# Kernel optimization log

Measured on AMD Instinct MI355X. Metric: run time of the kernel, lower is better.

The kernel has to match this reference:

```python
import jax, jax.numpy as jnp
import numpy as np

IGNORE_INDEX = -100


def setup_inputs() -> dict:
    key = jax.random.key(0)
    k1, k2, k3 = jax.random.split(key, 3)
    VOCAB, D = 32000, 2048
    B, S = 4, 2048
    weight = jax.random.normal(k1, (VOCAB, D), dtype=jnp.float32) * 0.02
    hidden = jax.random.normal(k2, (B, S, D), dtype=jnp.float32)
    targets = jax.random.randint(k3, (B, S), 0, VOCAB, dtype=jnp.int64)
    return {"weight": weight, "hidden": hidden, "targets": targets}


def reference(weight, hidden, targets):
    # Fused linear + cross-entropy: loss = sum_t CE(hidden_t @ W^T, target_t) / n_valid.
    # (The torch module chunks over sequence purely to save memory; the math is
    # identical to the unchunked computation below.)
    B, S, D = hidden.shape
    flat_h = hidden.reshape(-1, D)            # [B*S, D]
    flat_t = targets.reshape(-1)              # [B*S]
    logits = (flat_h @ weight.T).astype(jnp.float32)  # [B*S, V]
    lse = jax.nn.logsumexp(logits, axis=-1)   # [B*S]
    safe_t = jnp.clip(flat_t, 0, logits.shape[-1] - 1)
    tgt_logit = jnp.take_along_axis(logits, safe_t[:, None], axis=-1)[:, 0]
    valid = flat_t != IGNORE_INDEX
    per_tok = jnp.where(valid, lse - tgt_logit, 0.0)
    total_loss = per_tok.sum()
    n_valid = valid.sum().astype(jnp.float32)
    return jnp.where(n_valid > 0, total_loss / n_valid, total_loss)
```

## Files before the change

kernel.cpp:

```cpp
#include <hip/hip_runtime.h>

#define IGNORE_INDEX (-100)
#define VOCAB 32000
#define DDIM  2048
#define MTOK  8192

#define BM 128
#define BN 128
#define BK 128

#define WSCALE 32.0f
#define HSCALE 8.0f
#define INVSCALE (1.0f / 256.0f)
#define SCALE_ONE 0x7F7F7F7F

#define WBLK ((VOCAB * DDIM) / (256 * 16))
#define HBLK ((MTOK * DDIM) / (256 * 16))

typedef float f32x4 __attribute__((ext_vector_type(4)));
typedef int   i32x8 __attribute__((ext_vector_type(8)));
typedef unsigned char uchar_t;

__device__ __forceinline__ void cvt16(const float4* __restrict__ src,
                                      int4* __restrict__ dst, float scale,
                                      size_t i) {
    float4 a = src[4 * i], b = src[4 * i + 1], c = src[4 * i + 2], d = src[4 * i + 3];
    int4 o;
    int v;
    v = 0;
    v = __builtin_amdgcn_cvt_pk_fp8_f32(a.x * scale, a.y * scale, v, false);
    v = __builtin_amdgcn_cvt_pk_fp8_f32(a.z * scale, a.w * scale, v, true);
    o.x = v;
    v = 0;
    v = __builtin_amdgcn_cvt_pk_fp8_f32(b.x * scale, b.y * scale, v, false);
    v = __builtin_amdgcn_cvt_pk_fp8_f32(b.z * scale, b.w * scale, v, true);
    o.y = v;
    v = 0;
    v = __builtin_amdgcn_cvt_pk_fp8_f32(c.x * scale, c.y * scale, v, false);
    v = __builtin_amdgcn_cvt_pk_fp8_f32(c.z * scale, c.w * scale, v, true);
    o.z = v;
    v = 0;
    v = __builtin_amdgcn_cvt_pk_fp8_f32(d.x * scale, d.y * scale, v, false);
    v = __builtin_amdgcn_cvt_pk_fp8_f32(d.z * scale, d.w * scale, v, true);
    o.w = v;
    dst[i] = o;
}

__global__ void cvt_f32_fp8(const float4* __restrict__ srcW, int4* __restrict__ dstW,
                            const float4* __restrict__ srcH, int4* __restrict__ dstH) {
    if (blockIdx.x < WBLK) {
        size_t i = (size_t)blockIdx.x * blockDim.x + threadIdx.x;
        cvt16(srcW, dstW, WSCALE, i);
    } else {
        size_t i = (size_t)(blockIdx.x - WBLK) * blockDim.x + threadIdx.x;
        cvt16(srcH, dstH, HSCALE, i);
    }
}

__device__ __forceinline__ void load_lds16(const uchar_t* g, uchar_t* l) {
    __builtin_amdgcn_global_load_lds(
        (const __attribute__((address_space(1))) unsigned int*)(const void*)g,
        (__attribute__((address_space(3))) unsigned int*)(void*)l,
        16, 0, 0);
}

__global__ __launch_bounds__(256, 4) void gemm_ce(
    const uchar_t* __restrict__ A,
    const uchar_t* __restrict__ B,
    const int* __restrict__ targets,
    float* __restrict__ sumexp,
    float* __restrict__ tgtlogit) {
    __shared__ alignas(16) uchar_t As[BM * BK];
    __shared__ alignas(16) uchar_t Bs[BN * BK];

    const int tid  = threadIdx.x;
    const int wave = tid >> 6;
    const int lane = tid & 63;
    const int quad = lane >> 4;
    const int l16  = lane & 15;
    const int wm   = (wave >> 1) * 64;
    const int wn   = (wave & 1) * 64;

    const int m0 = blockIdx.x * BM;
    const int n0 = blockIdx.y * BN;

    const int srow = lane >> 3;
    const int scol = ((((lane & 7) >> 1) ^ (srow & 3)) << 5) + ((lane & 1) << 4);

    const uchar_t* Ap = A + (size_t)(m0 + wave * 32 + srow) * DDIM + scol;
    const uchar_t* Bp = B + (size_t)(n0 + wave * 32 + srow) * DDIM + scol;
    uchar_t* AsW = &As[(wave * 32) * BK];
    uchar_t* BsW = &Bs[(wave * 32) * BK];

    f32x4 acc[4][4];
    const f32x4 zero = {0.f, 0.f, 0.f, 0.f};
#pragma unroll
    for (int i = 0; i < 4; ++i)
#pragma unroll
        for (int j = 0; j < 4; ++j) acc[i][j] = zero;

#pragma clang loop unroll(disable)
    for (int k0 = 0; k0 < DDIM; k0 += BK) {
#pragma unroll
        for (int it = 0; it < 4; ++it) {
            load_lds16(Ap + (size_t)it * 8 * DDIM + k0, AsW + it * 8 * BK);
            load_lds16(Bp + (size_t)it * 8 * DDIM + k0, BsW + it * 8 * BK);
        }
        __syncthreads();

        const int gsw = ((quad ^ (l16 & 3)) << 5);
        i32x8 af[4];
#pragma unroll
        for (int i = 0; i < 4; ++i)
            af[i] = *reinterpret_cast<const i32x8*>(
                &As[(wm + i * 16 + l16) * BK + gsw]);
#pragma unroll
        for (int j = 0; j < 4; ++j) {
            const i32x8 bf = *reinterpret_cast<const i32x8*>(
                &Bs[(wn + j * 16 + l16) * BK + gsw]);
#pragma unroll
            for (int i = 0; i < 4; ++i)
                acc[i][j] = __builtin_amdgcn_mfma_scale_f32_16x16x128_f8f6f4(
                    af[i], bf, acc[i][j],
                    0 , 0 ,
                    0, SCALE_ONE, 0, SCALE_ONE);
        }
        __syncthreads();
    }

#pragma unroll
    for (int i = 0; i < 4; ++i) {
#pragma unroll
        for (int r = 0; r < 4; ++r) {
            const int mg = m0 + wm + i * 16 + quad * 4 + r;
            const int t  = targets[mg];
            float p = 0.f;
#pragma unroll
            for (int j = 0; j < 4; ++j) {
                float v = acc[i][j][r] * INVSCALE;
                p += __expf(v);
                if (t == n0 + wn + j * 16 + l16) tgtlogit[mg] = v;
            }
            p += __shfl_xor(p, 1);
            p += __shfl_xor(p, 2);
            p += __shfl_xor(p, 4);
            p += __shfl_xor(p, 8);
            if (l16 == 0) atomicAdd(&sumexp[mg], p);
        }
    }
}

__global__ void finalize(const float* __restrict__ sumexp,
                         const float* __restrict__ tgtlogit,
                         const int* __restrict__ targets,
                         float* __restrict__ out) {
    __shared__ float s_sum[8];
    __shared__ float s_cnt[8];
    float local = 0.f, cnt = 0.f;
    for (int t = threadIdx.x; t < MTOK; t += blockDim.x) {
        int tg = targets[t];
        if (tg != IGNORE_INDEX) {
            local += logf(sumexp[t]) - tgtlogit[t];
            cnt += 1.f;
        }
    }
#pragma unroll
    for (int o = 32; o > 0; o >>= 1) {
        local += __shfl_down(local, o);
        cnt   += __shfl_down(cnt, o);
    }
    const int wave = threadIdx.x >> 6, lane = threadIdx.x & 63;
    if (lane == 0) { s_sum[wave] = local; s_cnt[wave] = cnt; }
    __syncthreads();
    if (threadIdx.x == 0) {
        float ts = 0.f, tc = 0.f;
        for (int w = 0; w < (int)(blockDim.x >> 6); ++w) {
            ts += s_sum[w];
            tc += s_cnt[w];
        }
        out[0] = (tc > 0.f) ? (ts / tc) : ts;
    }
}

extern "C" void kernel_launch(void* const* d_in, const int* in_sizes, int n_in,
                              void* d_out, int out_size, void* d_ws,
                              size_t ws_size, hipStream_t stream) {
    const float* weight  = (const float*)d_in[0];
    const float* hidden  = (const float*)d_in[1];
    const int*   targets = (const int*)d_in[2];
    float* out = (float*)d_out;

    const size_t wbytes = (size_t)VOCAB * DDIM;
    const size_t hbytes = (size_t)MTOK * DDIM;
    uchar_t* Wb = (uchar_t*)d_ws;
    uchar_t* Hb = (uchar_t*)d_ws + wbytes;
    float* sumexp   = (float*)((char*)d_ws + wbytes + hbytes);
    float* tgtlogit = sumexp + MTOK;

    cvt_f32_fp8<<<WBLK + HBLK, 256, 0, stream>>>(
        (const float4*)weight, (int4*)Wb, (const float4*)hidden, (int4*)Hb);

    hipMemsetAsync(sumexp, 0, 2 * MTOK * sizeof(float), stream);

    dim3 grid(MTOK / BM, VOCAB / BN);
    gemm_ce<<<grid, 256, 0, stream>>>(Hb, Wb, targets, sumexp, tgtlogit);

    finalize<<<1, 512, 0, stream>>>(sumexp, tgtlogit, targets, out);
}
```

Baseline: 975.2 us.

## Triple-buffer LDS pipeline with 256x128 tiles, 8 waves, and block-level sumexp reduction

The GEMM moves to 256x128 tiles with 512 threads and a three-stage LDS ring. Global-to-LDS prefetch is issued two K-steps ahead and gated by explicit vmcnt waits and barriers, so memory latency overlaps the MFMAs. Other changes: a new 16-byte XOR swizzle with split fragment reads, s_setprio around the MFMA block, and an LDS reduction of per-row sumexp before one atomic per row. The memset is folded into the conversion kernel and finalize uses 1024 threads. LDS use rises to 144KB per block, which may cap occupancy at one block per CU despite launch_bounds(512,2).

```diff
diff --git a/kernel.cpp b/kernel.cpp
--- a/kernel.cpp
+++ b/kernel.cpp
@@ -5,9 +5,10 @@
 #define DDIM  2048
 #define MTOK  8192
 
-#define BM 128
+#define BM 256
 #define BN 128
 #define BK 128
+#define NKT (DDIM / BK)
 
 #define WSCALE 32.0f
 #define HSCALE 8.0f
@@ -16,6 +17,7 @@
 
 #define WBLK ((VOCAB * DDIM) / (256 * 16))
 #define HBLK ((MTOK * DDIM) / (256 * 16))
+#define ZBLK ((2 * MTOK * 4) / (256 * 16))
 
 typedef float f32x4 __attribute__((ext_vector_type(4)));
 typedef int   i32x8 __attribute__((ext_vector_type(8)));
@@ -47,13 +49,17 @@
 }
 
 __global__ void cvt_f32_fp8(const float4* __restrict__ srcW, int4* __restrict__ dstW,
-                            const float4* __restrict__ srcH, int4* __restrict__ dstH) {
+                            const float4* __restrict__ srcH, int4* __restrict__ dstH,
+                            int4* __restrict__ zr) {
     if (blockIdx.x < WBLK) {
         size_t i = (size_t)blockIdx.x * blockDim.x + threadIdx.x;
         cvt16(srcW, dstW, WSCALE, i);
-    } else {
+    } else if (blockIdx.x < WBLK + HBLK) {
         size_t i = (size_t)(blockIdx.x - WBLK) * blockDim.x + threadIdx.x;
         cvt16(srcH, dstH, HSCALE, i);
+    } else {
+        int i = (blockIdx.x - WBLK - HBLK) * 256 + threadIdx.x;
+        zr[i] = make_int4(0, 0, 0, 0);
     }
 }
 
@@ -64,14 +70,23 @@
         16, 0, 0);
 }
 
-__global__ __launch_bounds__(256, 4) void gemm_ce(
+__device__ __forceinline__ i32x8 read_frag(const uchar_t* arr, int off) {
+    int4 lo = *reinterpret_cast<const int4*>(arr + off);
+    int4 hi = *reinterpret_cast<const int4*>(arr + (off ^ 16));
+    i32x8 r;
+    r[0] = lo.x; r[1] = lo.y; r[2] = lo.z; r[3] = lo.w;
+    r[4] = hi.x; r[5] = hi.y; r[6] = hi.z; r[7] = hi.w;
+    return r;
+}
+
+__global__ __launch_bounds__(512, 2) void gemm_ce(
     const uchar_t* __restrict__ A,
     const uchar_t* __restrict__ B,
     const int* __restrict__ targets,
     float* __restrict__ sumexp,
     float* __restrict__ tgtlogit) {
-    __shared__ alignas(16) uchar_t As[BM * BK];
-    __shared__ alignas(16) uchar_t Bs[BN * BK];
+    __shared__ alignas(16) uchar_t As[3][BM * BK];
+    __shared__ alignas(16) uchar_t Bs[3][BN * BK];
 
     const int tid  = threadIdx.x;
     const int wave = tid >> 6;
@@ -85,12 +100,13 @@
     const int n0 = blockIdx.y * BN;
 
     const int srow = lane >> 3;
-    const int scol = ((((lane & 7) >> 1) ^ (srow & 3)) << 5) + ((lane & 1) << 4);
-
-    const uchar_t* Ap = A + (size_t)(m0 + wave * 32 + srow) * DDIM + scol;
-    const uchar_t* Bp = B + (size_t)(n0 + wave * 32 + srow) * DDIM + scol;
-    uchar_t* AsW = &As[(wave * 32) * BK];
-    uchar_t* BsW = &Bs[(wave * 32) * BK];
+    const int sswz = ((lane & 7) ^ srow) << 4;
+    const uchar_t* Ag = A + (size_t)(m0 + wave * 32 + srow) * DDIM + sswz;
+    const uchar_t* Bg = B + (size_t)(n0 + wave * 16 + srow) * DDIM + sswz;
+
+    const int swlo = ((quad << 1) ^ (l16 & 7)) << 4;
+    const int aoff = (wm + l16) * BK + swlo;
+    const int boff = (wn + l16) * BK + swlo;
 
     f32x4 acc[4][4];
     const f32x4 zero = {0.f, 0.f, 0.f, 0.f};
@@ -99,40 +115,70 @@
 #pragma unroll
         for (int j = 0; j < 4; ++j) acc[i][j] = zero;
 
+#define STAGE(buf, kk)                                                         \
+    do {                                                                       \
+        uchar_t* a_ = &As[0][0] + (buf) * (BM * BK) + (wave * 32) * BK;        \
+        uchar_t* b_ = &Bs[0][0] + (buf) * (BN * BK) + (wave * 16) * BK;        \
+        _Pragma("unroll") for (int it_ = 0; it_ < 4; ++it_)                    \
+            load_lds16(Ag + (size_t)it_ * 8 * DDIM + (kk), a_ + it_ * 8 * BK); \
+        _Pragma("unroll") for (int it_ = 0; it_ < 2; ++it_)                    \
+            load_lds16(Bg + (size_t)it_ * 8 * DDIM + (kk), b_ + it_ * 8 * BK); \
+    } while (0)
+
+#define COMPUTE(buf)                                                           \
+    do {                                                                       \
+        const uchar_t* as_ = &As[0][0] + (buf) * (BM * BK);                    \
+        const uchar_t* bs_ = &Bs[0][0] + (buf) * (BN * BK);                    \
+        i32x8 af[4], bf[4];                                                    \
+        _Pragma("unroll") for (int i_ = 0; i_ < 4; ++i_)                       \
+            af[i_] = read_frag(as_, aoff + i_ * 16 * BK);                      \
+        _Pragma("unroll") for (int j_ = 0; j_ < 4; ++j_)                       \
+            bf[j_] = read_frag(bs_, boff + j_ * 16 * BK);                      \
+        PREFETCH;                                                              \
+        __builtin_amdgcn_s_setprio(1);                                         \
+        _Pragma("unroll") for (int i_ = 0; i_ < 4; ++i_)                       \
+            _Pragma("unroll") for (int j_ = 0; j_ < 4; ++j_)                   \
+                acc[i_][j_] = __builtin_amdgcn_mfma_scale_f32_16x16x128_f8f6f4(\
+                    af[i_], bf[j_], acc[i_][j_],                               \
+                    0, 0, 0, SCALE_ONE, 0, SCALE_ONE);                         \
+        __builtin_amdgcn_s_setprio(0);                                         \
+    } while (0)
+
+#define VMCNT(n) asm volatile("s_waitcnt vmcnt(" #n ")" ::: "memory")
+#define BARRIER  asm volatile("s_barrier" ::: "memory")
+
+    STAGE(0, 0);
+    STAGE(1, BK);
+
+    int cur = 0, stg = 2;
 #pragma clang loop unroll(disable)
-    for (int k0 = 0; k0 < DDIM; k0 += BK) {
-#pragma unroll
-        for (int it = 0; it < 4; ++it) {
-            load_lds16(Ap + (size_t)it * 8 * DDIM + k0, AsW + it * 8 * BK);
-            load_lds16(Bp + (size_t)it * 8 * DDIM + k0, BsW + it * 8 * BK);
-        }
-        __syncthreads();
-
-        const int gsw = ((quad ^ (l16 & 3)) << 5);
-        i32x8 af[4];
-#pragma unroll
-        for (int i = 0; i < 4; ++i)
-            af[i] = *reinterpret_cast<const i32x8*>(
-                &As[(wm + i * 16 + l16) * BK + gsw]);
-#pragma unroll
-        for (int j = 0; j < 4; ++j) {
-            const i32x8 bf = *reinterpret_cast<const i32x8*>(
-                &Bs[(wn + j * 16 + l16) * BK + gsw]);
-#pragma unroll
-            for (int i = 0; i < 4; ++i)
-                acc[i][j] = __builtin_amdgcn_mfma_scale_f32_16x16x128_f8f6f4(
-                    af[i], bf, acc[i][j],
-                    0 , 0 ,
-                    0, SCALE_ONE, 0, SCALE_ONE);
-        }
-        __syncthreads();
-    }
-
+    for (int t = 0; t < NKT - 2; ++t) {
+        VMCNT(6);
+        BARRIER;
+#define PREFETCH STAGE(stg, (t + 2) * BK)
+        COMPUTE(cur);
+#undef PREFETCH
+        cur = (cur == 2) ? 0 : cur + 1;
+        stg = (stg == 2) ? 0 : stg + 1;
+    }
+#define PREFETCH
+    VMCNT(6);
+    BARRIER;
+    COMPUTE(cur);
+    cur = (cur == 2) ? 0 : cur + 1;
+    VMCNT(0);
+    BARRIER;
+    COMPUTE(cur);
+#undef PREFETCH
+
+    __syncthreads();
+    float* sred = reinterpret_cast<float*>(&As[0][0]);
 #pragma unroll
     for (int i = 0; i < 4; ++i) {
 #pragma unroll
         for (int r = 0; r < 4; ++r) {
-            const int mg = m0 + wm + i * 16 + quad * 4 + r;
+            const int rloc = wm + i * 16 + quad * 4 + r;
+            const int mg = m0 + rloc;
             const int t  = targets[mg];
             float p = 0.f;
 #pragma unroll
@@ -145,17 +191,27 @@
             p += __shfl_xor(p, 2);
             p += __shfl_xor(p, 4);
             p += __shfl_xor(p, 8);
-            if (l16 == 0) atomicAdd(&sumexp[mg], p);
+            if (l16 == 0) sred[(wave & 1) * 256 + rloc] = p;
         }
     }
+    __syncthreads();
+    if (tid < 256) {
+        float s = sred[tid] + sred[256 + tid];
+        atomicAdd(&sumexp[m0 + tid], s);
+    }
+
+#undef STAGE
+#undef COMPUTE
+#undef VMCNT
+#undef BARRIER
 }
 
 __global__ void finalize(const float* __restrict__ sumexp,
                          const float* __restrict__ tgtlogit,
                          const int* __restrict__ targets,
                          float* __restrict__ out) {
-    __shared__ float s_sum[8];
-    __shared__ float s_cnt[8];
+    __shared__ float s_sum[16];
+    __shared__ float s_cnt[16];
     float local = 0.f, cnt = 0.f;
     for (int t = threadIdx.x; t < MTOK; t += blockDim.x) {
         int tg = targets[t];
@@ -197,13 +253,12 @@
     float* sumexp   = (float*)((char*)d_ws + wbytes + hbytes);
     float* tgtlogit = sumexp + MTOK;
 
-    cvt_f32_fp8<<<WBLK + HBLK, 256, 0, stream>>>(
-        (const float4*)weight, (int4*)Wb, (const float4*)hidden, (int4*)Hb);
-
-    hipMemsetAsync(sumexp, 0, 2 * MTOK * sizeof(float), stream);
+    cvt_f32_fp8<<<WBLK + HBLK + ZBLK, 256, 0, stream>>>(
+        (const float4*)weight, (int4*)Wb, (const float4*)hidden, (int4*)Hb,
+        (int4*)sumexp);
 
     dim3 grid(MTOK / BM, VOCAB / BN);
-    gemm_ce<<<grid, 256, 0, stream>>>(Hb, Wb, targets, sumexp, tgtlogit);
-
-    finalize<<<1, 512, 0, stream>>>(sumexp, tgtlogit, targets, out);
-}
+    gemm_ce<<<grid, 512, 0, stream>>>(Hb, Wb, targets, sumexp, tgtlogit);
+
+    finalize<<<1, 1024, 0, stream>>>(sumexp, tgtlogit, targets, out);
+}
```

New measurement: 988.9 us. About the same (+1.4%).
